# Kernel optimization log

Hardware: AMD Instinct MI355X
Metric: run time of the kernel (lower is better)

## Reference

```python
import jax, jax.numpy as jnp
import numpy as np

N, D, K = 65536, 128, 4096
DECAY = 0.99
COMMIT_W = 1.0
EPS = 1e-5


def setup_inputs() -> dict:
    key = jax.random.key(0)
    k1, k2, k3 = jax.random.split(key, 3)
    x = jax.random.normal(k1, (N, D), dtype=jnp.float32)
    embed = jax.random.normal(k2, (K, D), dtype=jnp.float32)
    cluster_size = jnp.ones((K,), dtype=jnp.float32)
    embed_avg = jax.random.normal(k3, (K, D), dtype=jnp.float32)
    return {"x": x, "embed": embed, "cluster_size": cluster_size, "embed_avg": embed_avg}


def reference(x, embed, cluster_size, embed_avg):
    # --- codebook distance computation + argmin (torch.cdist(...).argmax(-dist)) ---
    x_sq = jnp.sum(x * x, axis=-1, keepdims=True)          # [N, 1]
    e_sq = jnp.sum(embed * embed, axis=-1)                 # [K]
    dist2 = x_sq - 2.0 * jnp.einsum("nd,kd->nk", x, embed) + e_sq  # [N, K]
    embed_ind = jnp.argmin(dist2, axis=-1)                 # [N] int

    # --- gather: quantize ---
    quantize = jnp.take(embed, embed_ind, axis=0)          # [N, D]

    # commitment loss (codes detached) + straight-through estimator
    commit_loss = COMMIT_W * jnp.mean(
        (jax.lax.stop_gradient(quantize) - x) ** 2
    )
    quantize_st = x + jax.lax.stop_gradient(quantize - x)

    # --- EMA codebook update (scatter_add / bincount pattern, no_grad) ---
    xs = jax.lax.stop_gradient(x)
    counts = jax.ops.segment_sum(
        jnp.ones((N,), dtype=jnp.float32), embed_ind, num_segments=K
    )                                                      # bincount [K]
    embed_sum = jax.ops.segment_sum(xs, embed_ind, num_segments=K)  # [K, D]

    new_cluster_size = cluster_size * DECAY + counts * (1.0 - DECAY)
    new_embed_avg = embed_avg * DECAY + embed_sum * (1.0 - DECAY)
    # laplace smoothing of cluster sizes
    n_total = jnp.sum(new_cluster_size)
    smoothed = (new_cluster_size + EPS) / (n_total + K * EPS) * n_total
    new_embed = new_embed_avg / smoothed[:, None]          # [K, D]

    return quantize_st, embed_ind, commit_loss, new_embed, new_cluster_size
```

## Files before the change

### kernel.cpp

```cpp
#include <hip/hip_runtime.h>
#include <math.h>

#define NPTS   65536
#define DIM    128
#define KCODES 4096

constexpr float DECAY_F         = 0.99f;
constexpr float ONE_MINUS_DECAY = 0.01f;
constexpr float EPS_F           = 1e-5f;

constexpr int OFF_IDX  = NPTS * DIM;
constexpr int OFF_LOSS = OFF_IDX + NPTS;
constexpr int OFF_EMB  = OFF_LOSS + 1;
constexpr int OFF_NCS  = OFF_EMB + KCODES * DIM;

typedef _Float16 half8 __attribute__((ext_vector_type(8)));
typedef _Float16 half4 __attribute__((ext_vector_type(4)));
typedef float    f32x4 __attribute__((ext_vector_type(4)));

__global__ __launch_bounds__(256) void vq_prep_kernel(const float* __restrict__ embed,
                                                      float* __restrict__ esq,
                                                      unsigned char* __restrict__ Eimg,
                                                      unsigned long long* __restrict__ rowpack,
                                                      unsigned int* __restrict__ counts,
                                                      float* __restrict__ esum,
                                                      float* __restrict__ out) {
    __shared__ float sq[512];
    int b = blockIdx.x, t = threadIdx.x;

    rowpack[b * 512 + t]       = ~0ULL;
    rowpack[b * 512 + 256 + t] = ~0ULL;
    if (t < 32) counts[b * 32 + t] = 0u;
    if (b == 0 && t == 0) out[OFF_LOSS] = 0.f;

    {
        float4* ez = (float4*)esum;
#pragma unroll
        for (int j = 0; j < 4; ++j) ez[(size_t)b * 1024 + j * 256 + t] = (float4){0.f, 0.f, 0.f, 0.f};
    }

    unsigned char* img = Eimg + ((size_t)b << 14);
#pragma unroll
    for (int it = 0; it < 2; ++it) {
        int idx = t + it * 256;
        int r = idx >> 4, c8 = idx & 15;
        const float4* src = (const float4*)(embed + (size_t)(b * 32 + r) * DIM + c8 * 8);
        float4 v0 = src[0], v1 = src[1];
        float e[8] = {v0.x, v0.y, v0.z, v0.w, v1.x, v1.y, v1.z, v1.w};
        half8 h8, l8;
        float ss = 0.f;
#pragma unroll
        for (int j = 0; j < 8; ++j) {
            _Float16 h = (_Float16)e[j];
            h8[j] = h;
            l8[j] = (_Float16)(e[j] - (float)h);
            ss = fmaf(e[j], e[j], ss);
        }
        int bo = r * 256 + ((c8 * 16) ^ ((r & 7) << 4));
        *(half8*)(img + bo)        = h8;
        *(half8*)(img + 8192 + bo) = l8;
        sq[idx] = ss;
    }
    __syncthreads();
    if (t < 32) {
        float s = 0.f;
#pragma unroll
        for (int c = 0; c < 16; ++c) s += sq[t * 16 + c];
        esq[b * 32 + t] = s;
    }
}

__global__ __launch_bounds__(256, 4)
void vq_main_kernel(const float* __restrict__ x, const float* __restrict__ esq,
                    const unsigned char* __restrict__ Eimg,
                    unsigned long long* __restrict__ rowpack,
                    unsigned int* __restrict__ counts,
                    int* __restrict__ sidx,
                    float* __restrict__ out) {
    __shared__ __align__(16) unsigned char lds[40960];

    const int tid  = threadIdx.x;
    const int l    = tid & 63;
    const int w    = tid >> 6;
    const int mblk = blockIdx.x >> 1;
    const int half = blockIdx.x & 1;
    const int row0 = mblk * 128;

    {
        const float4* eq = (const float4*)(esq + half * 2048);
        float4* dst = (float4*)(lds + 32768);
        dst[tid]       = eq[tid];
        dst[tid + 256] = eq[tid + 256];
    }

    half8 ahi[2][4], alo[2][4];
#pragma unroll
    for (int ph = 0; ph < 2; ++ph) {
        if (ph) __syncthreads();
        const float4* xg = (const float4*)(x + (size_t)(row0 + ph * 64) * DIM);
#pragma unroll
        for (int it = 0; it < 8; ++it) {
            int i4 = tid + it * 256;
            int r = i4 >> 5, c4 = i4 & 31;
            float4 v = xg[i4];
            float m0 = -2.f * v.x, m1 = -2.f * v.y, m2 = -2.f * v.z, m3 = -2.f * v.w;
            half4 h, lo;
            h[0] = (_Float16)m0; h[1] = (_Float16)m1; h[2] = (_Float16)m2; h[3] = (_Float16)m3;
            lo[0] = (_Float16)(m0 - (float)h[0]); lo[1] = (_Float16)(m1 - (float)h[1]);
            lo[2] = (_Float16)(m2 - (float)h[2]); lo[3] = (_Float16)(m3 - (float)h[3]);
            int bo = r * 256 + ((c4 * 8) ^ ((r & 7) << 4));
            *(half4*)(lds + bo)         = h;
            *(half4*)(lds + 16384 + bo) = lo;
        }
        __syncthreads();
        if ((w >> 1) == ph) {
#pragma unroll
            for (int rf = 0; rf < 2; ++rf)
#pragma unroll
                for (int ks = 0; ks < 4; ++ks) {
                    int rloc = (w & 1) * 32 + rf * 16 + (l & 15);
                    int bo = rloc * 256 + ((ks * 64 + (l >> 4) * 16) ^ ((rloc & 7) << 4));
                    ahi[rf][ks] = *(const half8*)(lds + bo);
                    alo[rf][ks] = *(const half8*)(lds + 16384 + bo);
                }
        }
    }
    __syncthreads();

#define STAGE(P, CT)                                                                     \
    {                                                                                    \
        const unsigned char* gsrc = Eimg + ((size_t)(half * 64 + (CT)) << 14);           \
        _Pragma("unroll")                                                                \
        for (int t = 0; t < 4; ++t) {                                                    \
            __builtin_amdgcn_global_load_lds(                                            \
                (const __attribute__((address_space(1))) unsigned int*)(gsrc + t * 4096 + w * 1024 + l * 16), \
                (__attribute__((address_space(3))) unsigned int*)(lds + (P) * 16384 + t * 4096 + w * 1024),   \
                16, 0, 0);                                                               \
        }                                                                                \
    }

    float minv[2][4];
    int   mini[2][4];
#pragma unroll
    for (int rf = 0; rf < 2; ++rf)
#pragma unroll
        for (int r = 0; r < 4; ++r) { minv[rf][r] = 3.4e38f; mini[rf][r] = 0; }

    const float* esql = (const float*)(lds + 32768);
    STAGE(0, 0);

    for (int ct = 0; ct < 64; ++ct) {
        const int p = ct & 1;
        if (ct < 63) {
            STAGE(p ^ 1, ct + 1);
            asm volatile("s_waitcnt vmcnt(4)" ::: "memory");
        } else {
            asm volatile("s_waitcnt vmcnt(0)" ::: "memory");
        }
        __builtin_amdgcn_s_barrier();

        const unsigned char* bb = lds + p * 16384;

        float ecf[2];
        ecf[0] = esql[ct * 32 + (l & 15)];
        ecf[1] = esql[ct * 32 + 16 + (l & 15)];

        f32x4 acc[2][2];
#pragma unroll
        for (int rf = 0; rf < 2; ++rf)
#pragma unroll
            for (int cf = 0; cf < 2; ++cf) {
                float e = ecf[cf];
                acc[rf][cf] = (f32x4){e, e, e, e};
            }

        __builtin_amdgcn_s_setprio(1);
#pragma unroll
        for (int ks = 0; ks < 4; ++ks) {
#pragma unroll
            for (int cf = 0; cf < 2; ++cf) {
                int rowb = cf * 16 + (l & 15);
                int bo = rowb * 256 + ((ks * 64 + (l >> 4) * 16) ^ ((rowb & 7) << 4));
                half8 bh = *(const half8*)(bb + bo);
                half8 bl = *(const half8*)(bb + 8192 + bo);
                acc[0][cf] = __builtin_amdgcn_mfma_f32_16x16x32_f16(ahi[0][ks], bh, acc[0][cf], 0, 0, 0);
                acc[1][cf] = __builtin_amdgcn_mfma_f32_16x16x32_f16(ahi[1][ks], bh, acc[1][cf], 0, 0, 0);
                acc[0][cf] = __builtin_amdgcn_mfma_f32_16x16x32_f16(alo[0][ks], bh, acc[0][cf], 0, 0, 0);
                acc[1][cf] = __builtin_amdgcn_mfma_f32_16x16x32_f16(alo[1][ks], bh, acc[1][cf], 0, 0, 0);
                acc[0][cf] = __builtin_amdgcn_mfma_f32_16x16x32_f16(ahi[0][ks], bl, acc[0][cf], 0, 0, 0);
                acc[1][cf] = __builtin_amdgcn_mfma_f32_16x16x32_f16(ahi[1][ks], bl, acc[1][cf], 0, 0, 0);
            }
        }
        __builtin_amdgcn_s_setprio(0);

#pragma unroll
        for (int rf = 0; rf < 2; ++rf)
#pragma unroll
            for (int cf = 0; cf < 2; ++cf) {
                int kidx = half * 2048 + ct * 32 + cf * 16 + (l & 15);
#pragma unroll
                for (int r = 0; r < 4; ++r) {
                    float v = acc[rf][cf][r];
                    if (v < minv[rf][r]) { minv[rf][r] = v; mini[rf][r] = kidx; }
                }
            }

        __builtin_amdgcn_s_barrier();
    }

#pragma unroll
    for (int off = 1; off < 16; off <<= 1) {
#pragma unroll
        for (int rf = 0; rf < 2; ++rf)
#pragma unroll
            for (int r = 0; r < 4; ++r) {
                float v2 = __shfl_xor(minv[rf][r], off);
                int   i2 = __shfl_xor(mini[rf][r], off);
                if (v2 < minv[rf][r] || (v2 == minv[rf][r] && i2 < mini[rf][r])) {
                    minv[rf][r] = v2; mini[rf][r] = i2;
                }
            }
    }
    if ((l & 15) == 0) {
#pragma unroll
        for (int rf = 0; rf < 2; ++rf)
#pragma unroll
            for (int r = 0; r < 4; ++r) {
                int row = row0 + w * 32 + rf * 16 + (l >> 4) * 4 + r;
                unsigned int u = __float_as_uint(minv[rf][r]);
                u = (u & 0x80000000u) ? ~u : (u | 0x80000000u);
                unsigned long long key = ((unsigned long long)u << 32) | (unsigned int)mini[rf][r];
                unsigned long long old = atomicMin(&rowpack[row], key);
                if (old != ~0ULL) {
                    unsigned long long fin = old < key ? old : key;
                    int kf = (int)(fin & 0xFFFFFFFFu);
                    out[OFF_IDX + row] = (float)kf;
                    sidx[row] = kf;
                    atomicAdd(&counts[kf], 1u);
                }
            }
    }
}

__global__ __launch_bounds__(256) void vq_scan_kernel(const unsigned int* __restrict__ counts,
                                                      const float* __restrict__ cs,
                                                      float* __restrict__ out,
                                                      int* __restrict__ offsets,
                                                      int* __restrict__ cursor,
                                                      float* __restrict__ inv_sm) {
    __shared__ int   wsum[4];
    __shared__ float wnsum[4];
    int tid = threadIdx.x, l = tid & 63, w = tid >> 6;

    unsigned int c[16];
    float vl[16];
    int   csum = 0;
    float nsum = 0.f;
#pragma unroll
    for (int j = 0; j < 16; ++j) {
        int i = tid * 16 + j;
        c[j] = counts[i];
        csum += (int)c[j];
        float v = fmaf(cs[i], DECAY_F, (float)c[j] * ONE_MINUS_DECAY);
        vl[j] = v;
        nsum += v;
        out[OFF_NCS + i] = v;
    }

    int inc = csum;
#pragma unroll
    for (int off = 1; off < 64; off <<= 1) {
        int t = __shfl_up(inc, off);
        if (l >= off) inc += t;
    }
    float nred = nsum;
#pragma unroll
    for (int off = 32; off >= 1; off >>= 1) nred += __shfl_xor(nred, off);

    if (l == 63) wsum[w] = inc;
    if (l == 0)  wnsum[w] = nred;
    __syncthreads();

    int wpre = 0;
    for (int i = 0; i < w; ++i) wpre += wsum[i];
    float ntot = wnsum[0] + wnsum[1] + wnsum[2] + wnsum[3];
    float num  = ntot + (float)KCODES * EPS_F;

    int off_ = wpre + inc - csum;
#pragma unroll
    for (int j = 0; j < 16; ++j) {
        int i = tid * 16 + j;
        offsets[i] = off_;
        cursor[i]  = off_;
        off_ += (int)c[j];
        inv_sm[i] = num / ((vl[j] + EPS_F) * ntot);
    }
}

__global__ __launch_bounds__(256) void vq_sort_kernel(const int* __restrict__ sidx,
                                                      int* __restrict__ cursor,
                                                      int* __restrict__ rowids,
                                                      int* __restrict__ skey) {
    int r = blockIdx.x * 256 + threadIdx.x;
    int k = sidx[r];
    int pos = atomicAdd(&cursor[k], 1);
    rowids[pos] = r;
    skey[pos]   = k;
}

__global__ __launch_bounds__(256) void vq_segsum_kernel(const float* __restrict__ x,
                                                        const float* __restrict__ embed,
                                                        const int* __restrict__ rowids,
                                                        const int* __restrict__ skey,
                                                        const int* __restrict__ offsets,
                                                        const unsigned int* __restrict__ counts,
                                                        float* __restrict__ esum,
                                                        float* __restrict__ out) {
    __shared__ float buck[64][DIM];
    __shared__ int   rid_s[64], rank_s[64], bcode_s[64];
    __shared__ int   nseg_s;
    __shared__ float lred[4];

    const int tid = threadIdx.x;
    const int w   = tid >> 6, l = tid & 63;
    const int p0  = blockIdx.x * 64;

    {
        float4* bz = (float4*)&buck[0][0];
#pragma unroll
        for (int j = 0; j < 8; ++j) bz[j * 256 + tid] = (float4){0.f, 0.f, 0.f, 0.f};
    }

    if (tid < 64) {
        int p = p0 + tid;
        int k = skey[p];
        rid_s[tid] = rowids[p];
        int f = (tid == 0) ? 1 : (k != skey[p - 1] ? 1 : 0);
        int inc = f;
#pragma unroll
        for (int off = 1; off < 64; off <<= 1) {
            int t = __shfl_up(inc, off);
            if (tid >= off) inc += t;
        }
        int rank = inc - 1;
        rank_s[tid] = rank;
        if (f) bcode_s[rank] = k;
        if (tid == 63) nseg_s = inc;
    }
    __syncthreads();

    float lsum = 0.f;
    {
        int prevb = rank_s[w * 16];
        float2 ev = *(const float2*)(embed + (size_t)bcode_s[prevb] * DIM + l * 2);
        float ra0 = 0.f, ra1 = 0.f;
#pragma unroll 4
        for (int i = 0; i < 16; ++i) {
            int pl = w * 16 + i;
            int r  = rid_s[pl];
            int b  = rank_s[pl];
            if (b != prevb) {
                atomicAdd(&buck[prevb][l * 2],     ra0);
                atomicAdd(&buck[prevb][l * 2 + 1], ra1);
                ra0 = 0.f; ra1 = 0.f;
                prevb = b;
                ev = *(const float2*)(embed + (size_t)bcode_s[b] * DIM + l * 2);
            }
            float2 xv = *(const float2*)(x + (size_t)r * DIM + l * 2);
            *(float2*)(out + (size_t)r * DIM + l * 2) = ev;
            ra0 += xv.x; ra1 += xv.y;
            float d0 = ev.x - xv.x, d1 = ev.y - xv.y;
            lsum = fmaf(d0, d0, fmaf(d1, d1, lsum));
        }
        atomicAdd(&buck[prevb][l * 2],     ra0);
        atomicAdd(&buck[prevb][l * 2 + 1], ra1);
    }

#pragma unroll
    for (int s = 32; s >= 1; s >>= 1) lsum += __shfl_xor(lsum, s);
    if (l == 0) lred[w] = lsum;
    __syncthreads();

    int nseg = nseg_s;
    for (int b = w; b < nseg; b += 4) {
        int kb = bcode_s[b];
        int o  = offsets[kb];
        int c  = (int)counts[kb];
        float v0 = buck[b][l * 2], v1 = buck[b][l * 2 + 1];
        if (o >= p0 && o + c <= p0 + 64) {
            *(float2*)(esum + (size_t)kb * DIM + l * 2) = (float2){v0, v1};
        } else {
            atomicAdd(esum + (size_t)kb * DIM + l * 2,     v0);
            atomicAdd(esum + (size_t)kb * DIM + l * 2 + 1, v1);
        }
    }

    if (tid == 0) {
        float bl = (lred[0] + lred[1]) + (lred[2] + lred[3]);
        atomicAdd(out + OFF_LOSS, bl * (1.0f / ((float)NPTS * (float)DIM)));
    }
}

__global__ __launch_bounds__(256) void vq_embed_kernel(const float* __restrict__ eavg,
                                                       const float* __restrict__ esum,
                                                       const float* __restrict__ inv_sm,
                                                       float* __restrict__ out) {
    int i = blockIdx.x * 256 + threadIdx.x;
    int k = i >> 7;
    out[OFF_EMB + i] = fmaf(eavg[i], DECAY_F, esum[i] * ONE_MINUS_DECAY) * inv_sm[k];
}

extern "C" void kernel_launch(void* const* d_in, const int* in_sizes, int n_in,
                              void* d_out, int out_size, void* d_ws, size_t ws_size,
                              hipStream_t stream) {
    const float* x     = (const float*)d_in[0];
    const float* embed = (const float*)d_in[1];
    const float* cs    = (const float*)d_in[2];
    const float* eavg  = (const float*)d_in[3];
    float* out = (float*)d_out;

    unsigned long long* rowpack = (unsigned long long*)d_ws;
    float*         esq     = (float*)(rowpack + NPTS);
    float*         inv_sm  = esq + KCODES;
    unsigned int*  counts  = (unsigned int*)(inv_sm + KCODES);
    int*           offsets = (int*)(counts + KCODES);
    int*           cursor  = offsets + KCODES;
    int*           rowids  = cursor + KCODES;
    int*           sidx    = rowids + NPTS;
    int*           skey    = sidx + NPTS;
    float*         esum    = (float*)(skey + NPTS);
    unsigned char* Eimg    = (unsigned char*)(esum + KCODES * DIM);

    vq_prep_kernel<<<KCODES / 32, 256, 0, stream>>>(embed, esq, Eimg, rowpack, counts, esum, out);
    vq_main_kernel<<<NPTS / 128 * 2, 256, 0, stream>>>(x, esq, Eimg, rowpack, counts, sidx, out);
    vq_scan_kernel<<<1, 256, 0, stream>>>(counts, cs, out, offsets, cursor, inv_sm);
    vq_sort_kernel<<<NPTS / 256, 256, 0, stream>>>(sidx, cursor, rowids, skey);
    vq_segsum_kernel<<<NPTS / 64, 256, 0, stream>>>(x, embed, rowids, skey, offsets, counts, esum, out);
    vq_embed_kernel<<<(KCODES * DIM) / 256, 256, 0, stream>>>(eavg, esum, inv_sm, out);
}
```

Measured before the change: 222.2 us.

## Switch distance GEMM to 32x32x16 MFMA with dual accumulators

Replaces the 16x16x32 f16 MFMA tiling (2x2 fragments per wave) with a single 32x32x16 MFMA tile per wave, using two 16-wide accumulators to split the hi/lo compensated products into independent dependency chains. The A fragments, LDS read addressing, per-row argmin bookkeeping and the cross-lane reduction (now over 32 lanes) are remapped to the 32x32 output layout. Occupancy hint drops from 4 to 3 blocks per CU to accommodate the larger accumulator register footprint. The aim is higher MFMA throughput and fewer LDS B-fragment reads per tile, at the cost of more registers and a longer reduction.

New measurement: 271.9 us. 1.22x slower.

```diff
diff --git a/kernel.cpp b/kernel.cpp
--- a/kernel.cpp
+++ b/kernel.cpp
@@ -16,7 +16,7 @@
 
 typedef _Float16 half8 __attribute__((ext_vector_type(8)));
 typedef _Float16 half4 __attribute__((ext_vector_type(4)));
-typedef float    f32x4 __attribute__((ext_vector_type(4)));
+typedef float    f32x16 __attribute__((ext_vector_type(16)));
 
 __global__ __launch_bounds__(256) void vq_prep_kernel(const float* __restrict__ embed,
                                                       float* __restrict__ esq,
@@ -70,7 +70,7 @@
     }
 }
 
-__global__ __launch_bounds__(256, 4)
+__global__ __launch_bounds__(256, 3)
 void vq_main_kernel(const float* __restrict__ x, const float* __restrict__ esq,
                     const unsigned char* __restrict__ Eimg,
                     unsigned long long* __restrict__ rowpack,
@@ -82,6 +82,8 @@
     const int tid  = threadIdx.x;
     const int l    = tid & 63;
     const int w    = tid >> 6;
+    const int c31  = l & 31;
+    const int h2   = l >> 5;
     const int mblk = blockIdx.x >> 1;
     const int half = blockIdx.x & 1;
     const int row0 = mblk * 128;
@@ -93,7 +95,7 @@
         dst[tid + 256] = eq[tid + 256];
     }
 
-    half8 ahi[2][4], alo[2][4];
+    half8 ahi[8], alo[8];
 #pragma unroll
     for (int ph = 0; ph < 2; ++ph) {
         if (ph) __syncthreads();
@@ -114,15 +116,13 @@
         }
         __syncthreads();
         if ((w >> 1) == ph) {
-#pragma unroll
-            for (int rf = 0; rf < 2; ++rf)
-#pragma unroll
-                for (int ks = 0; ks < 4; ++ks) {
-                    int rloc = (w & 1) * 32 + rf * 16 + (l & 15);
-                    int bo = rloc * 256 + ((ks * 64 + (l >> 4) * 16) ^ ((rloc & 7) << 4));
-                    ahi[rf][ks] = *(const half8*)(lds + bo);
-                    alo[rf][ks] = *(const half8*)(lds + 16384 + bo);
-                }
+            int rloc = (w & 1) * 32 + c31;
+#pragma unroll
+            for (int ks = 0; ks < 8; ++ks) {
+                int bo = rloc * 256 + ((ks * 32 + h2 * 16) ^ ((rloc & 7) << 4));
+                ahi[ks] = *(const half8*)(lds + bo);
+                alo[ks] = *(const half8*)(lds + 16384 + bo);
+            }
         }
     }
     __syncthreads();
@@ -139,12 +139,10 @@
         }                                                                                \
     }
 
-    float minv[2][4];
-    int   mini[2][4];
-#pragma unroll
-    for (int rf = 0; rf < 2; ++rf)
-#pragma unroll
-        for (int r = 0; r < 4; ++r) { minv[rf][r] = 3.4e38f; mini[rf][r] = 0; }
+    float minv[16];
+    int   mini[16];
+#pragma unroll
+    for (int j = 0; j < 16; ++j) { minv[j] = 3.4e38f; mini[j] = 0; }
 
     const float* esql = (const float*)(lds + 32768);
     STAGE(0, 0);
@@ -161,84 +159,61 @@
 
         const unsigned char* bb = lds + p * 16384;
 
-        float ecf[2];
-        ecf[0] = esql[ct * 32 + (l & 15)];
-        ecf[1] = esql[ct * 32 + 16 + (l & 15)];
-
-        f32x4 acc[2][2];
-#pragma unroll
-        for (int rf = 0; rf < 2; ++rf)
-#pragma unroll
-            for (int cf = 0; cf < 2; ++cf) {
-                float e = ecf[cf];
-                acc[rf][cf] = (f32x4){e, e, e, e};
+        float e = esql[ct * 32 + c31];
+        f32x16 acc1, acc2;
+#pragma unroll
+        for (int j = 0; j < 16; ++j) { acc1[j] = e; acc2[j] = 0.f; }
+
+        __builtin_amdgcn_s_setprio(1);
+#pragma unroll
+        for (int ks = 0; ks < 8; ++ks) {
+            int bo = c31 * 256 + ((ks * 32 + h2 * 16) ^ ((c31 & 7) << 4));
+            half8 bh = *(const half8*)(bb + bo);
+            half8 bl = *(const half8*)(bb + 8192 + bo);
+            acc1 = __builtin_amdgcn_mfma_f32_32x32x16_f16(ahi[ks], bh, acc1, 0, 0, 0);
+            acc2 = __builtin_amdgcn_mfma_f32_32x32x16_f16(alo[ks], bh, acc2, 0, 0, 0);
+            if (ks & 1)
+                acc2 = __builtin_amdgcn_mfma_f32_32x32x16_f16(ahi[ks], bl, acc2, 0, 0, 0);
+            else
+                acc1 = __builtin_amdgcn_mfma_f32_32x32x16_f16(ahi[ks], bl, acc1, 0, 0, 0);
+        }
+        __builtin_amdgcn_s_setprio(0);
+
+        int kidx = half * 2048 + ct * 32 + c31;
+#pragma unroll
+        for (int j = 0; j < 16; ++j) {
+            float v = acc1[j] + acc2[j];
+            if (v < minv[j]) { minv[j] = v; mini[j] = kidx; }
+        }
+
+        __builtin_amdgcn_s_barrier();
+    }
+
+#pragma unroll
+    for (int off = 1; off < 32; off <<= 1) {
+#pragma unroll
+        for (int j = 0; j < 16; ++j) {
+            float v2 = __shfl_xor(minv[j], off);
+            int   i2 = __shfl_xor(mini[j], off);
+            if (v2 < minv[j] || (v2 == minv[j] && i2 < mini[j])) { minv[j] = v2; mini[j] = i2; }
+        }
+    }
+    if (c31 == 0) {
+#pragma unroll
+        for (int j = 0; j < 16; ++j) {
+            int row = row0 + w * 32 + (j & 3) + 8 * (j >> 2) + 4 * h2;
+            unsigned int u = __float_as_uint(minv[j]);
+            u = (u & 0x80000000u) ? ~u : (u | 0x80000000u);
+            unsigned long long key = ((unsigned long long)u << 32) | (unsigned int)mini[j];
+            unsigned long long old = atomicMin(&rowpack[row], key);
+            if (old != ~0ULL) {
+                unsigned long long fin = old < key ? old : key;
+                int kf = (int)(fin & 0xFFFFFFFFu);
+                out[OFF_IDX + row] = (float)kf;
+                sidx[row] = kf;
+                atomicAdd(&counts[kf], 1u);
             }
-
-        __builtin_amdgcn_s_setprio(1);
-#pragma unroll
-        for (int ks = 0; ks < 4; ++ks) {
-#pragma unroll
-            for (int cf = 0; cf < 2; ++cf) {
-                int rowb = cf * 16 + (l & 15);
-                int bo = rowb * 256 + ((ks * 64 + (l >> 4) * 16) ^ ((rowb & 7) << 4));
-                half8 bh = *(const half8*)(bb + bo);
-                half8 bl = *(const half8*)(bb + 8192 + bo);
-                acc[0][cf] = __builtin_amdgcn_mfma_f32_16x16x32_f16(ahi[0][ks], bh, acc[0][cf], 0, 0, 0);
-                acc[1][cf] = __builtin_amdgcn_mfma_f32_16x16x32_f16(ahi[1][ks], bh, acc[1][cf], 0, 0, 0);
-                acc[0][cf] = __builtin_amdgcn_mfma_f32_16x16x32_f16(alo[0][ks], bh, acc[0][cf], 0, 0, 0);
-                acc[1][cf] = __builtin_amdgcn_mfma_f32_16x16x32_f16(alo[1][ks], bh, acc[1][cf], 0, 0, 0);
-                acc[0][cf] = __builtin_amdgcn_mfma_f32_16x16x32_f16(ahi[0][ks], bl, acc[0][cf], 0, 0, 0);
-                acc[1][cf] = __builtin_amdgcn_mfma_f32_16x16x32_f16(ahi[1][ks], bl, acc[1][cf], 0, 0, 0);
-            }
-        }
-        __builtin_amdgcn_s_setprio(0);
-
-#pragma unroll
-        for (int rf = 0; rf < 2; ++rf)
-#pragma unroll
-            for (int cf = 0; cf < 2; ++cf) {
-                int kidx = half * 2048 + ct * 32 + cf * 16 + (l & 15);
-#pragma unroll
-                for (int r = 0; r < 4; ++r) {
-                    float v = acc[rf][cf][r];
-                    if (v < minv[rf][r]) { minv[rf][r] = v; mini[rf][r] = kidx; }
-                }
-            }
-
-        __builtin_amdgcn_s_barrier();
-    }
-
-#pragma unroll
-    for (int off = 1; off < 16; off <<= 1) {
-#pragma unroll
-        for (int rf = 0; rf < 2; ++rf)
-#pragma unroll
-            for (int r = 0; r < 4; ++r) {
-                float v2 = __shfl_xor(minv[rf][r], off);
-                int   i2 = __shfl_xor(mini[rf][r], off);
-                if (v2 < minv[rf][r] || (v2 == minv[rf][r] && i2 < mini[rf][r])) {
-                    minv[rf][r] = v2; mini[rf][r] = i2;
-                }
-            }
-    }
-    if ((l & 15) == 0) {
-#pragma unroll
-        for (int rf = 0; rf < 2; ++rf)
-#pragma unroll
-            for (int r = 0; r < 4; ++r) {
-                int row = row0 + w * 32 + rf * 16 + (l >> 4) * 4 + r;
-                unsigned int u = __float_as_uint(minv[rf][r]);
-                u = (u & 0x80000000u) ? ~u : (u | 0x80000000u);
-                unsigned long long key = ((unsigned long long)u << 32) | (unsigned int)mini[rf][r];
-                unsigned long long old = atomicMin(&rowpack[row], key);
-                if (old != ~0ULL) {
-                    unsigned long long fin = old < key ? old : key;
-                    int kf = (int)(fin & 0xFFFFFFFFu);
-                    out[OFF_IDX + row] = (float)kf;
-                    sidx[row] = kf;
-                    atomicAdd(&counts[kf], 1u);
-                }
-            }
+        }
     }
 }
 
```
